# Kernel tuning notes

Measured on AMD Instinct MI355X. Metric: run time of the kernel, lower is better.

The kernel has to match this reference:

```python
import jax, jax.numpy as jnp
import numpy as np

N, E, D = 50000, 600000, 128
EPS = 1e-6


def setup_inputs() -> dict:
    key = jax.random.key(0)
    ks = jax.random.split(key, 16)
    scale = 1.0 / np.sqrt(D)
    inp = {
        "h": jax.random.normal(ks[0], (N, D), dtype=jnp.float32),
        "e": jax.random.normal(ks[1], (E, D), dtype=jnp.float32),
        "src": jax.random.randint(ks[2], (E,), 0, N, dtype=jnp.int32),
        "dst": jax.random.randint(ks[3], (E,), 0, N, dtype=jnp.int32),
    }
    for i, name in enumerate(["A", "B", "C", "D", "E"]):
        inp[f"W{name}"] = jax.random.uniform(ks[4 + 2 * i], (D, D), dtype=jnp.float32, minval=-scale, maxval=scale)
        inp[f"b{name}"] = jax.random.uniform(ks[5 + 2 * i], (D,), dtype=jnp.float32, minval=-scale, maxval=scale)
    return inp


def reference(h, e, src, dst, WA, bA, WB, bB, WC, bC, WD, bD, WE, bE):
    h_in, e_in = h, e
    Ah = h @ WA.T + bA            # [N, D]
    Bh = h @ WB.T + bB
    Dh = h @ WD.T + bD
    Eh = h @ WE.T + bE
    Ce = e @ WC.T + bC            # [E, D]
    # edge update: e' = Dh[u] + Eh[v] + Ce
    e_new = Dh[src] + Eh[dst] + Ce              # [E, D]
    sigma = jax.nn.sigmoid(e_new)               # [E, D]
    msg = Bh[src] * sigma                        # [E, D]
    sum_sigma_h = jax.ops.segment_sum(msg, dst, num_segments=N)    # [N, D]
    sum_sigma = jax.ops.segment_sum(sigma, dst, num_segments=N)    # [N, D]
    h_new = Ah + sum_sigma_h / (sum_sigma + EPS)
    h_out = h_in + jax.nn.silu(h_new)   # residual (input_dim == output_dim)
    e_out = e_in + jax.nn.silu(e_new)
    return h_out, e_out
```

## Files before the change

kernel.cpp:

```cpp
#include <hip/hip_runtime.h>
#include <hip/hip_bf16.h>

#define N_NODES 50000
#define N_EDGES 600000
#define DD 128
#define EPS 1e-6f

#define NBLK_SCAN 196
#define CNT_LEN   (NBLK_SCAN*256)

typedef __bf16 bf16;
typedef __attribute__((ext_vector_type(8))) __bf16 bf16x8;
typedef __attribute__((ext_vector_type(4))) float f32x4;

__device__ __forceinline__ f32x4 mfma16(bf16x8 a, bf16x8 b, f32x4 c) {
    return __builtin_amdgcn_mfma_f32_16x16x32_bf16(a, b, c, 0, 0, 0);
}

__device__ __forceinline__ int wave_incl_scan(int v, int lane) {
#pragma unroll
    for (int ofs = 1; ofs < 64; ofs <<= 1) {
        int t = __shfl_up(v, ofs, 64);
        if (lane >= ofs) v += t;
    }
    return v;
}

__global__ void conv_w_kernel(const float* __restrict__ WA, const float* __restrict__ WB,
                              const float* __restrict__ WC, const float* __restrict__ WD,
                              const float* __restrict__ WE, bf16* __restrict__ out) {
    int i = blockIdx.x * 256 + threadIdx.x;
    const float* srcs[5] = {WA, WB, WC, WD, WE};
    int w = i >> 14;
    int j = i & 16383;
    out[i] = (bf16)srcs[w][j];
}

__global__ void hist_kernel(const int* __restrict__ dst, int* __restrict__ cnt) {
    int i = blockIdx.x * 256 + threadIdx.x;
    if (i < N_EDGES) atomicAdd(&cnt[dst[i]], 1);
}

__global__ __launch_bounds__(256) void scan_a_kernel(const int* __restrict__ cnt,
                                                     int* __restrict__ dpos,
                                                     int* __restrict__ bsum) {
    __shared__ int wsum[4];
    int tid = threadIdx.x, lane = tid & 63, wv = tid >> 6;
    int i = blockIdx.x * 256 + tid;
    int v = (i < N_NODES) ? cnt[i] : 0;
    int s = wave_incl_scan(v, lane);
    if (lane == 63) wsum[wv] = s;
    __syncthreads();
    int woff = 0;
#pragma unroll
    for (int w = 0; w < 3; ++w) if (w < wv) woff += wsum[w];
    if (i < N_NODES) dpos[i] = woff + s - v;
    if (tid == 255) bsum[blockIdx.x] = woff + s;
}

__global__ __launch_bounds__(256) void scan_b_kernel(int* __restrict__ bsum) {
    __shared__ int wsum[4];
    int tid = threadIdx.x, lane = tid & 63, wv = tid >> 6;
    int v = (tid < NBLK_SCAN) ? bsum[tid] : 0;
    int s = wave_incl_scan(v, lane);
    if (lane == 63) wsum[wv] = s;
    __syncthreads();
    int woff = 0;
#pragma unroll
    for (int w = 0; w < 3; ++w) if (w < wv) woff += wsum[w];
    if (tid < NBLK_SCAN) bsum[tid] = woff + s - v;
}

__global__ void scan_c_kernel(int* __restrict__ dpos, const int* __restrict__ bsum) {
    int i = blockIdx.x * 256 + threadIdx.x;
    if (i < N_NODES) dpos[i] += bsum[blockIdx.x];
}

__global__ void scatter_kernel(const int* __restrict__ dst, int* __restrict__ dpos,
                               int* __restrict__ perm) {
    int i = blockIdx.x * 256 + threadIdx.x;
    if (i < N_EDGES) {
        int p = atomicAdd(&dpos[dst[i]], 1);
        perm[p] = i;
    }
}

__global__ __launch_bounds__(256) void node_gemm_kernel(
    const float* __restrict__ h, const bf16* __restrict__ Wb,
    const float* __restrict__ bA, const float* __restrict__ bB,
    const float* __restrict__ bD, const float* __restrict__ bE,
    bf16* __restrict__ Ah, bf16* __restrict__ Bh,
    bf16* __restrict__ Dh, bf16* __restrict__ Eh)
{
    __shared__ bf16 hs[64 * 136];
    int tid = threadIdx.x;
    int n0 = blockIdx.x * 64;

#pragma unroll
    for (int it = 0; it < 8; ++it) {
        int idx = it * 256 + tid;
        int row = idx >> 5;
        int c4  = idx & 31;
        int grow = n0 + row;
        if (grow >= N_NODES) grow = N_NODES - 1;
        float4 v = ((const float4*)h)[grow * 32 + c4];
        bf16* d = &hs[row * 136 + c4 * 4];
        d[0] = (bf16)v.x; d[1] = (bf16)v.y; d[2] = (bf16)v.z; d[3] = (bf16)v.w;
    }
    __syncthreads();

    int lane = tid & 63, wv = tid >> 6;
    int l15 = lane & 15, quad = lane >> 4;

    const bf16* Wsel[4] = {Wb, Wb + 16384, Wb + 3 * 16384, Wb + 4 * 16384};
    const float* bsel[4] = {bA, bB, bD, bE};
    bf16* osel[4] = {Ah, Bh, Dh, Eh};

#pragma unroll 1
    for (int wi = 0; wi < 4; ++wi) {
        const bf16* W = Wsel[wi];
        f32x4 acc[4][2] = {};
#pragma unroll
        for (int ks = 0; ks < 4; ++ks) {
            int kk = ks * 32 + quad * 8;
            bf16x8 b0 = *(const bf16x8*)&W[((2 * wv) * 16 + l15) * 128 + kk];
            bf16x8 b1 = *(const bf16x8*)&W[((2 * wv + 1) * 16 + l15) * 128 + kk];
#pragma unroll
            for (int mt = 0; mt < 4; ++mt) {
                bf16x8 a = *(const bf16x8*)&hs[(mt * 16 + l15) * 136 + kk];
                acc[mt][0] = mfma16(a, b0, acc[mt][0]);
                acc[mt][1] = mfma16(a, b1, acc[mt][1]);
            }
        }
#pragma unroll
        for (int nt = 0; nt < 2; ++nt) {
            int col = (2 * wv + nt) * 16 + l15;
            float bias = bsel[wi][col];
#pragma unroll
            for (int mt = 0; mt < 4; ++mt) {
#pragma unroll
                for (int r = 0; r < 4; ++r) {
                    int row = mt * 16 + quad * 4 + r;
                    int grow = n0 + row;
                    if (grow < N_NODES)
                        osel[wi][grow * 128 + col] = (bf16)(acc[mt][nt][r] + bias);
                }
            }
        }
    }
}

__global__ __launch_bounds__(256) void edge_kernel(
    const float* __restrict__ e, const int* __restrict__ src, const int* __restrict__ dst,
    const int* __restrict__ perm,
    const bf16* __restrict__ WCb, const float* __restrict__ bC,
    const bf16* __restrict__ Bh, const bf16* __restrict__ Dh, const bf16* __restrict__ Eh,
    float* __restrict__ sum_sigma, float* __restrict__ sum_msg,
    float* __restrict__ e_out)
{
    __shared__ bf16 es[64 * 136];
    __shared__ int s_ei[64];
    __shared__ int s_src[64];
    __shared__ int s_dst[64];
    int tid = threadIdx.x;
    int e0 = blockIdx.x * 64;

    if (tid < 64) {
        int p = perm[e0 + tid];
        s_ei[tid]  = p;
        s_src[tid] = src[p];
        s_dst[tid] = dst[p];
    }
    __syncthreads();

#pragma unroll
    for (int it = 0; it < 8; ++it) {
        int idx = it * 256 + tid;
        int row = idx >> 5;
        int c4  = idx & 31;
        float4 v = ((const float4*)e)[s_ei[row] * 32 + c4];
        bf16* d = &es[row * 136 + c4 * 4];
        d[0] = (bf16)v.x; d[1] = (bf16)v.y; d[2] = (bf16)v.z; d[3] = (bf16)v.w;
    }
    __syncthreads();

    int lane = tid & 63, wv = tid >> 6;
    int l15 = lane & 15, quad = lane >> 4;

    f32x4 acc[4][2] = {};
#pragma unroll
    for (int ks = 0; ks < 4; ++ks) {
        int kk = ks * 32 + quad * 8;
        bf16x8 b0 = *(const bf16x8*)&WCb[((2 * wv) * 16 + l15) * 128 + kk];
        bf16x8 b1 = *(const bf16x8*)&WCb[((2 * wv + 1) * 16 + l15) * 128 + kk];
#pragma unroll
        for (int mt = 0; mt < 4; ++mt) {
            bf16x8 a = *(const bf16x8*)&es[(mt * 16 + l15) * 136 + kk];
            acc[mt][0] = mfma16(a, b0, acc[mt][0]);
            acc[mt][1] = mfma16(a, b1, acc[mt][1]);
        }
    }

#pragma unroll
    for (int nt = 0; nt < 2; ++nt) {
        int col = (2 * wv + nt) * 16 + l15;
        float bc = bC[col];
#pragma unroll
        for (int mt = 0; mt < 4; ++mt) {
            float a_sg = 0.f, a_ms = 0.f;
            int prev = -1;
#pragma unroll
            for (int r = 0; r < 4; ++r) {
                int row = mt * 16 + quad * 4 + r;
                int ei = s_ei[row];
                int s  = s_src[row];
                int dd = s_dst[row];
                float dh = (float)Dh[s * 128 + col];
                float eh = (float)Eh[dd * 128 + col];
                float bh = (float)Bh[s * 128 + col];
                float enew = acc[mt][nt][r] + bc + dh + eh;
                float sg = 1.0f / (1.0f + __expf(-enew));
                float ein = e[(size_t)ei * 128 + col];
                e_out[(size_t)ei * 128 + col] = ein + enew * sg;
                if (dd != prev && prev >= 0) {
                    unsafeAtomicAdd(&sum_sigma[prev * 128 + col], a_sg);
                    unsafeAtomicAdd(&sum_msg[prev * 128 + col], a_ms);
                    a_sg = 0.f; a_ms = 0.f;
                }
                a_sg += sg;
                a_ms += bh * sg;
                prev = dd;
            }
            unsafeAtomicAdd(&sum_sigma[prev * 128 + col], a_sg);
            unsafeAtomicAdd(&sum_msg[prev * 128 + col], a_ms);
        }
    }
}

__global__ void node_final_kernel(const float* __restrict__ h, const bf16* __restrict__ Ah,
                                  const float* __restrict__ sum_sigma,
                                  const float* __restrict__ sum_msg,
                                  float* __restrict__ h_out)
{
    int i = blockIdx.x * 256 + threadIdx.x;
    if (i < N_NODES * DD) {
        float hn = (float)Ah[i] + sum_msg[i] / (sum_sigma[i] + EPS);
        float sg = 1.0f / (1.0f + __expf(-hn));
        h_out[i] = h[i] + hn * sg;
    }
}

extern "C" void kernel_launch(void* const* d_in, const int* in_sizes, int n_in,
                              void* d_out, int out_size, void* d_ws, size_t ws_size,
                              hipStream_t stream) {
    const float* h   = (const float*)d_in[0];
    const float* e   = (const float*)d_in[1];
    const int*   src = (const int*)d_in[2];
    const int*   dst = (const int*)d_in[3];
    const float* WA = (const float*)d_in[4];  const float* bA = (const float*)d_in[5];
    const float* WB = (const float*)d_in[6];  const float* bB = (const float*)d_in[7];
    const float* WC = (const float*)d_in[8];  const float* bC = (const float*)d_in[9];
    const float* WD = (const float*)d_in[10]; const float* bD = (const float*)d_in[11];
    const float* WE = (const float*)d_in[12]; const float* bE = (const float*)d_in[13];

    float* h_out = (float*)d_out;
    float* e_out = h_out + (size_t)N_NODES * DD;

    char* ws = (char*)d_ws;
    bf16* Wb = (bf16*)ws;            ws += (size_t)5 * 16384 * sizeof(bf16);
    bf16* Ah = (bf16*)ws;            ws += (size_t)N_NODES * DD * sizeof(bf16);
    bf16* Bh = (bf16*)ws;            ws += (size_t)N_NODES * DD * sizeof(bf16);
    bf16* Dh = (bf16*)ws;            ws += (size_t)N_NODES * DD * sizeof(bf16);
    bf16* Eh = (bf16*)ws;            ws += (size_t)N_NODES * DD * sizeof(bf16);
    float* sum_sigma = (float*)ws;   ws += (size_t)N_NODES * DD * sizeof(float);
    float* sum_msg   = (float*)ws;   ws += (size_t)N_NODES * DD * sizeof(float);
    int* counts = (int*)ws;          ws += (size_t)CNT_LEN * sizeof(int);
    int* dpos   = (int*)ws;          ws += (size_t)CNT_LEN * sizeof(int);
    int* bsum   = (int*)ws;          ws += (size_t)256 * sizeof(int);
    int* perm   = (int*)ws;          ws += (size_t)N_EDGES * sizeof(int);

    hipMemsetAsync(sum_sigma, 0,
                   (size_t)2 * N_NODES * DD * sizeof(float) + (size_t)CNT_LEN * sizeof(int),
                   stream);

    conv_w_kernel<<<320, 256, 0, stream>>>(WA, WB, WC, WD, WE, Wb);

    hist_kernel<<<(N_EDGES + 255) / 256, 256, 0, stream>>>(dst, counts);
    scan_a_kernel<<<NBLK_SCAN, 256, 0, stream>>>(counts, dpos, bsum);
    scan_b_kernel<<<1, 256, 0, stream>>>(bsum);
    scan_c_kernel<<<NBLK_SCAN, 256, 0, stream>>>(dpos, bsum);
    scatter_kernel<<<(N_EDGES + 255) / 256, 256, 0, stream>>>(dst, dpos, perm);

    node_gemm_kernel<<<(N_NODES + 63) / 64, 256, 0, stream>>>(
        h, Wb, bA, bB, bD, bE, Ah, Bh, Dh, Eh);
    edge_kernel<<<N_EDGES / 64, 256, 0, stream>>>(
        e, src, dst, perm, Wb + 2 * 16384, bC, Bh, Dh, Eh, sum_sigma, sum_msg, e_out);
    node_final_kernel<<<(N_NODES * DD + 255) / 256, 256, 0, stream>>>(
        h, Ah, sum_sigma, sum_msg, h_out);
}
```

Before: 1.085 ms.

## Replace atomic segment sums with CSR gather aggregation over dst-sorted sigma buffer

The edge kernel now processes edges in their original order, so reads of e and writes of e_out are coalesced. It writes sigma as bf16 into a buffer permuted into dst-sorted order instead of doing float atomics into node accumulators. A new node aggregation kernel walks each node's CSR range, gathers Bh[src] and sigma, reduces both sums in registers, and fuses the final silu residual. This removes the large memset and the atomic traffic, but it adds an intermediate buffer of E×D bf16 (about 150 MB written and then read back) and rounds sigma to bf16 before the reduction.

```diff
diff --git a/kernel.cpp b/kernel.cpp
--- a/kernel.cpp
+++ b/kernel.cpp
@@ -11,6 +11,7 @@
 
 typedef __bf16 bf16;
 typedef __attribute__((ext_vector_type(8))) __bf16 bf16x8;
+typedef __attribute__((ext_vector_type(4))) __bf16 bf16x4;
 typedef __attribute__((ext_vector_type(4))) float f32x4;
 
 __device__ __forceinline__ f32x4 mfma16(bf16x8 a, bf16x8 b, f32x4 c) {
@@ -30,10 +31,12 @@
                               const float* __restrict__ WC, const float* __restrict__ WD,
                               const float* __restrict__ WE, bf16* __restrict__ out) {
     int i = blockIdx.x * 256 + threadIdx.x;
-    const float* srcs[5] = {WA, WB, WC, WD, WE};
     int w = i >> 14;
     int j = i & 16383;
-    out[i] = (bf16)srcs[w][j];
+    const float* s;
+    if (w == 0) s = WA; else if (w == 1) s = WB; else if (w == 2) s = WC;
+    else if (w == 3) s = WD; else s = WE;
+    out[i] = (bf16)s[j];
 }
 
 __global__ void hist_kernel(const int* __restrict__ dst, int* __restrict__ cnt) {
@@ -71,17 +74,24 @@
     if (tid < NBLK_SCAN) bsum[tid] = woff + s - v;
 }
 
-__global__ void scan_c_kernel(int* __restrict__ dpos, const int* __restrict__ bsum) {
+__global__ void scan_c_kernel(int* __restrict__ dpos, const int* __restrict__ bsum,
+                              int* __restrict__ spos) {
     int i = blockIdx.x * 256 + threadIdx.x;
-    if (i < N_NODES) dpos[i] += bsum[blockIdx.x];
-}
-
-__global__ void scatter_kernel(const int* __restrict__ dst, int* __restrict__ dpos,
-                               int* __restrict__ perm) {
+    if (i < N_NODES) {
+        int v = dpos[i] + bsum[blockIdx.x];
+        dpos[i] = v;
+        spos[i] = v;
+    }
+}
+
+__global__ void scatter_kernel(const int* __restrict__ src, const int* __restrict__ dst,
+                               int* __restrict__ spos,
+                               int* __restrict__ srcs_sorted, int* __restrict__ inv) {
     int i = blockIdx.x * 256 + threadIdx.x;
     if (i < N_EDGES) {
-        int p = atomicAdd(&dpos[dst[i]], 1);
-        perm[p] = i;
+        int p = atomicAdd(&spos[dst[i]], 1);
+        srcs_sorted[p] = src[i];
+        inv[i] = p;
     }
 }
 
@@ -104,21 +114,21 @@
         int grow = n0 + row;
         if (grow >= N_NODES) grow = N_NODES - 1;
         float4 v = ((const float4*)h)[grow * 32 + c4];
-        bf16* d = &hs[row * 136 + c4 * 4];
-        d[0] = (bf16)v.x; d[1] = (bf16)v.y; d[2] = (bf16)v.z; d[3] = (bf16)v.w;
+        bf16x4 p; p[0] = (bf16)v.x; p[1] = (bf16)v.y; p[2] = (bf16)v.z; p[3] = (bf16)v.w;
+        *(bf16x4*)&hs[row * 136 + c4 * 4] = p;
     }
     __syncthreads();
 
     int lane = tid & 63, wv = tid >> 6;
     int l15 = lane & 15, quad = lane >> 4;
 
-    const bf16* Wsel[4] = {Wb, Wb + 16384, Wb + 3 * 16384, Wb + 4 * 16384};
-    const float* bsel[4] = {bA, bB, bD, bE};
-    bf16* osel[4] = {Ah, Bh, Dh, Eh};
-
 #pragma unroll 1
     for (int wi = 0; wi < 4; ++wi) {
-        const bf16* W = Wsel[wi];
+        const bf16* W; const float* bias; bf16* out;
+        if (wi == 0)      { W = Wb;             bias = bA; out = Ah; }
+        else if (wi == 1) { W = Wb + 16384;     bias = bB; out = Bh; }
+        else if (wi == 2) { W = Wb + 3 * 16384; bias = bD; out = Dh; }
+        else              { W = Wb + 4 * 16384; bias = bE; out = Eh; }
         f32x4 acc[4][2] = {};
 #pragma unroll
         for (int ks = 0; ks < 4; ++ks) {
@@ -135,7 +145,7 @@
 #pragma unroll
         for (int nt = 0; nt < 2; ++nt) {
             int col = (2 * wv + nt) * 16 + l15;
-            float bias = bsel[wi][col];
+            float bias_v = bias[col];
 #pragma unroll
             for (int mt = 0; mt < 4; ++mt) {
 #pragma unroll
@@ -143,7 +153,7 @@
                     int row = mt * 16 + quad * 4 + r;
                     int grow = n0 + row;
                     if (grow < N_NODES)
-                        osel[wi][grow * 128 + col] = (bf16)(acc[mt][nt][r] + bias);
+                        out[grow * 128 + col] = (bf16)(acc[mt][nt][r] + bias_v);
                 }
             }
         }
@@ -152,35 +162,30 @@
 
 __global__ __launch_bounds__(256) void edge_kernel(
     const float* __restrict__ e, const int* __restrict__ src, const int* __restrict__ dst,
-    const int* __restrict__ perm,
+    const int* __restrict__ inv,
     const bf16* __restrict__ WCb, const float* __restrict__ bC,
-    const bf16* __restrict__ Bh, const bf16* __restrict__ Dh, const bf16* __restrict__ Eh,
-    float* __restrict__ sum_sigma, float* __restrict__ sum_msg,
-    float* __restrict__ e_out)
+    const bf16* __restrict__ Dh, const bf16* __restrict__ Eh,
+    bf16* __restrict__ sgb, float* __restrict__ e_out)
 {
     __shared__ bf16 es[64 * 136];
-    __shared__ int s_ei[64];
     __shared__ int s_src[64];
     __shared__ int s_dst[64];
+    __shared__ int s_pos[64];
     int tid = threadIdx.x;
     int e0 = blockIdx.x * 64;
 
-    if (tid < 64) {
-        int p = perm[e0 + tid];
-        s_ei[tid]  = p;
-        s_src[tid] = src[p];
-        s_dst[tid] = dst[p];
-    }
-    __syncthreads();
+    if (tid < 64)        s_src[tid]       = src[e0 + tid];
+    else if (tid < 128)  s_dst[tid - 64]  = dst[e0 + tid - 64];
+    else if (tid < 192)  s_pos[tid - 128] = inv[e0 + tid - 128];
 
 #pragma unroll
     for (int it = 0; it < 8; ++it) {
         int idx = it * 256 + tid;
         int row = idx >> 5;
         int c4  = idx & 31;
-        float4 v = ((const float4*)e)[s_ei[row] * 32 + c4];
-        bf16* d = &es[row * 136 + c4 * 4];
-        d[0] = (bf16)v.x; d[1] = (bf16)v.y; d[2] = (bf16)v.z; d[3] = (bf16)v.w;
+        float4 v = ((const float4*)e)[(e0 + row) * 32 + c4];
+        bf16x4 p; p[0] = (bf16)v.x; p[1] = (bf16)v.y; p[2] = (bf16)v.z; p[3] = (bf16)v.w;
+        *(bf16x4*)&es[row * 136 + c4 * 4] = p;
     }
     __syncthreads();
 
@@ -207,47 +212,87 @@
         float bc = bC[col];
 #pragma unroll
         for (int mt = 0; mt < 4; ++mt) {
-            float a_sg = 0.f, a_ms = 0.f;
-            int prev = -1;
 #pragma unroll
             for (int r = 0; r < 4; ++r) {
                 int row = mt * 16 + quad * 4 + r;
-                int ei = s_ei[row];
+                int ei = e0 + row;
                 int s  = s_src[row];
                 int dd = s_dst[row];
+                int ps = s_pos[row];
                 float dh = (float)Dh[s * 128 + col];
                 float eh = (float)Eh[dd * 128 + col];
-                float bh = (float)Bh[s * 128 + col];
                 float enew = acc[mt][nt][r] + bc + dh + eh;
                 float sg = 1.0f / (1.0f + __expf(-enew));
                 float ein = e[(size_t)ei * 128 + col];
                 e_out[(size_t)ei * 128 + col] = ein + enew * sg;
-                if (dd != prev && prev >= 0) {
-                    unsafeAtomicAdd(&sum_sigma[prev * 128 + col], a_sg);
-                    unsafeAtomicAdd(&sum_msg[prev * 128 + col], a_ms);
-                    a_sg = 0.f; a_ms = 0.f;
-                }
-                a_sg += sg;
-                a_ms += bh * sg;
-                prev = dd;
+                sgb[(size_t)ps * 128 + col] = (bf16)sg;
             }
-            unsafeAtomicAdd(&sum_sigma[prev * 128 + col], a_sg);
-            unsafeAtomicAdd(&sum_msg[prev * 128 + col], a_ms);
-        }
-    }
-}
-
-__global__ void node_final_kernel(const float* __restrict__ h, const bf16* __restrict__ Ah,
-                                  const float* __restrict__ sum_sigma,
-                                  const float* __restrict__ sum_msg,
-                                  float* __restrict__ h_out)
+        }
+    }
+}
+
+__global__ __launch_bounds__(256) void node_agg_kernel(
+    const int* __restrict__ rstart, const int* __restrict__ cnt,
+    const int* __restrict__ srcs_sorted,
+    const bf16* __restrict__ sgb, const bf16* __restrict__ Bh,
+    const bf16* __restrict__ Ah, const float* __restrict__ h,
+    float* __restrict__ h_out)
 {
-    int i = blockIdx.x * 256 + threadIdx.x;
-    if (i < N_NODES * DD) {
-        float hn = (float)Ah[i] + sum_msg[i] / (sum_sigma[i] + EPS);
-        float sg = 1.0f / (1.0f + __expf(-hn));
-        h_out[i] = h[i] + hn * sg;
-    }
+    int tid = threadIdx.x;
+    int g = tid >> 4, c = tid & 15;
+    int n = blockIdx.x * 16 + g;
+
+    int beg = rstart[n];
+    int deg = cnt[n];
+
+    float ssg[8] = {0.f, 0.f, 0.f, 0.f, 0.f, 0.f, 0.f, 0.f};
+    float sms[8] = {0.f, 0.f, 0.f, 0.f, 0.f, 0.f, 0.f, 0.f};
+
+    int j = 0;
+    for (; j + 1 < deg; j += 2) {
+        int s0 = srcs_sorted[beg + j];
+        int s1 = srcs_sorted[beg + j + 1];
+        bf16x8 g0 = *(const bf16x8*)&sgb[(size_t)(beg + j) * 128 + c * 8];
+        bf16x8 g1 = *(const bf16x8*)&sgb[(size_t)(beg + j + 1) * 128 + c * 8];
+        bf16x8 b0 = *(const bf16x8*)&Bh[(size_t)s0 * 128 + c * 8];
+        bf16x8 b1 = *(const bf16x8*)&Bh[(size_t)s1 * 128 + c * 8];
+#pragma unroll
+        for (int k = 0; k < 8; ++k) {
+            float v0 = (float)g0[k], v1 = (float)g1[k];
+            ssg[k] += v0 + v1;
+            sms[k] += v0 * (float)b0[k] + v1 * (float)b1[k];
+        }
+    }
+    if (j < deg) {
+        int s0 = srcs_sorted[beg + j];
+        bf16x8 g0 = *(const bf16x8*)&sgb[(size_t)(beg + j) * 128 + c * 8];
+        bf16x8 b0 = *(const bf16x8*)&Bh[(size_t)s0 * 128 + c * 8];
+#pragma unroll
+        for (int k = 0; k < 8; ++k) {
+            float v0 = (float)g0[k];
+            ssg[k] += v0;
+            sms[k] += v0 * (float)b0[k];
+        }
+    }
+
+    bf16x8 a8 = *(const bf16x8*)&Ah[(size_t)n * 128 + c * 8];
+    const float4* h4 = (const float4*)h;
+    float4 hv0 = h4[n * 32 + c * 2];
+    float4 hv1 = h4[n * 32 + c * 2 + 1];
+
+    float o[8];
+#pragma unroll
+    for (int k = 0; k < 8; ++k) {
+        float hn = (float)a8[k] + sms[k] / (ssg[k] + EPS);
+        float sig = 1.0f / (1.0f + __expf(-hn));
+        o[k] = hn * sig;
+    }
+    float4 r0, r1;
+    r0.x = hv0.x + o[0]; r0.y = hv0.y + o[1]; r0.z = hv0.z + o[2]; r0.w = hv0.w + o[3];
+    r1.x = hv1.x + o[4]; r1.y = hv1.y + o[5]; r1.z = hv1.z + o[6]; r1.w = hv1.w + o[7];
+    float4* o4 = (float4*)h_out;
+    o4[n * 32 + c * 2]     = r0;
+    o4[n * 32 + c * 2 + 1] = r1;
 }
 
 extern "C" void kernel_launch(void* const* d_in, const int* in_sizes, int n_in,
@@ -272,29 +317,28 @@
     bf16* Bh = (bf16*)ws;            ws += (size_t)N_NODES * DD * sizeof(bf16);
     bf16* Dh = (bf16*)ws;            ws += (size_t)N_NODES * DD * sizeof(bf16);
     bf16* Eh = (bf16*)ws;            ws += (size_t)N_NODES * DD * sizeof(bf16);
-    float* sum_sigma = (float*)ws;   ws += (size_t)N_NODES * DD * sizeof(float);
-    float* sum_msg   = (float*)ws;   ws += (size_t)N_NODES * DD * sizeof(float);
+    bf16* sgb = (bf16*)ws;           ws += (size_t)N_EDGES * DD * sizeof(bf16);
     int* counts = (int*)ws;          ws += (size_t)CNT_LEN * sizeof(int);
     int* dpos   = (int*)ws;          ws += (size_t)CNT_LEN * sizeof(int);
+    int* spos   = (int*)ws;          ws += (size_t)CNT_LEN * sizeof(int);
     int* bsum   = (int*)ws;          ws += (size_t)256 * sizeof(int);
-    int* perm   = (int*)ws;          ws += (size_t)N_EDGES * sizeof(int);
-
-    hipMemsetAsync(sum_sigma, 0,
-                   (size_t)2 * N_NODES * DD * sizeof(float) + (size_t)CNT_LEN * sizeof(int),
-                   stream);
+    int* srcs_sorted = (int*)ws;     ws += (size_t)N_EDGES * sizeof(int);
+    int* inv    = (int*)ws;          ws += (size_t)N_EDGES * sizeof(int);
+
+    hipMemsetAsync(counts, 0, (size_t)CNT_LEN * sizeof(int), stream);
 
     conv_w_kernel<<<320, 256, 0, stream>>>(WA, WB, WC, WD, WE, Wb);
 
     hist_kernel<<<(N_EDGES + 255) / 256, 256, 0, stream>>>(dst, counts);
     scan_a_kernel<<<NBLK_SCAN, 256, 0, stream>>>(counts, dpos, bsum);
     scan_b_kernel<<<1, 256, 0, stream>>>(bsum);
-    scan_c_kernel<<<NBLK_SCAN, 256, 0, stream>>>(dpos, bsum);
-    scatter_kernel<<<(N_EDGES + 255) / 256, 256, 0, stream>>>(dst, dpos, perm);
+    scan_c_kernel<<<NBLK_SCAN, 256, 0, stream>>>(dpos, bsum, spos);
+    scatter_kernel<<<(N_EDGES + 255) / 256, 256, 0, stream>>>(src, dst, spos, srcs_sorted, inv);
 
     node_gemm_kernel<<<(N_NODES + 63) / 64, 256, 0, stream>>>(
         h, Wb, bA, bB, bD, bE, Ah, Bh, Dh, Eh);
     edge_kernel<<<N_EDGES / 64, 256, 0, stream>>>(
-        e, src, dst, perm, Wb + 2 * 16384, bC, Bh, Dh, Eh, sum_sigma, sum_msg, e_out);
-    node_final_kernel<<<(N_NODES * DD + 255) / 256, 256, 0, stream>>>(
-        h, Ah, sum_sigma, sum_msg, h_out);
-}
+        e, src, dst, inv, Wb + 2 * 16384, bC, Dh, Eh, sgb, e_out);
+    node_agg_kernel<<<N_NODES / 16, 256, 0, stream>>>(
+        dpos, counts, srcs_sorted, sgb, Bh, Ah, h, h_out);
+}
```

After: 873.4 us. -19.5%, faster.
